# Optimization experiments

Measured on AMD Instinct MI355X. Metric: run time of the kernel, lower is better.

Reference implementation:

```python
import jax, jax.numpy as jnp
import numpy as np

NUM_GENS = 1024
N = 8388608

def setup_inputs() -> dict:
    key = jax.random.key(0)
    k1, k2, k3, k4, k5, k6, k7, k8 = jax.random.split(key, 8)
    return {
        "x_gen": jax.random.randint(k1, (N,), 0, NUM_GENS, dtype=jnp.int64 if jax.config.jax_enable_x64 else jnp.int32),
        "x_ix": jax.random.randint(k2, (N,), 0, NUM_GENS, dtype=jnp.int64 if jax.config.jax_enable_x64 else jnp.int32),
        "x_max_clock_speed": jax.random.normal(k3, (N,), dtype=jnp.float32),
        "x_max_tdp": jax.random.normal(k4, (N,), dtype=jnp.float32),
        "gen_map": jax.random.normal(k5, (NUM_GENS,), dtype=jnp.float32),
        "b": jax.random.normal(k6, (), dtype=jnp.float32),
        "c": jax.random.normal(k7, (), dtype=jnp.float32),
        "d": jax.random.normal(k8, (), dtype=jnp.float32),
    }

def reference(x_gen, x_ix, x_max_clock_speed, x_max_tdp, gen_map, b, c, d):
    # sum(one_hot(x_gen, G) * gen_map, 1) is mathematically gen_map[x_gen]
    gathered = jnp.take(gen_map, x_gen, axis=0)  # [N]
    return gathered + c * x_max_clock_speed + d * x_max_tdp
```

## Files before the change

### kernel.cpp

```cpp
#include <hip/hip_runtime.h>


#define NUM_GENS 1024
#define BLOCK 256
#define GRID 1024
#define UNROLL 4

typedef float nfloat4 __attribute__((ext_vector_type(4)));
typedef int   nint4   __attribute__((ext_vector_type(4)));

__device__ __forceinline__ nfloat4 stage_compute(const float* s_map, float c, float d,
                                                 nint4 g, nfloat4 a, nfloat4 b) {
    nfloat4 o;
    o.x = s_map[g.x] + c * a.x + d * b.x;
    o.y = s_map[g.y] + c * a.y + d * b.y;
    o.z = s_map[g.z] + c * a.z + d * b.z;
    o.w = s_map[g.w] + c * a.w + d * b.w;
    return o;
}

__global__ __launch_bounds__(BLOCK, 4)
void Model_64364379898151_kernel(const int* __restrict__ x_gen,
                                 const float* __restrict__ x_clock,
                                 const float* __restrict__ x_tdp,
                                 const float* __restrict__ gen_map,
                                 const float* __restrict__ c_ptr,
                                 const float* __restrict__ d_ptr,
                                 float* __restrict__ out,
                                 int n_vec)
{
    __shared__ float s_map[NUM_GENS];
    ((float4*)s_map)[threadIdx.x] = ((const float4*)gen_map)[threadIdx.x];
    __syncthreads();

    const float c = c_ptr[0];
    const float d = d_ptr[0];

    const int stride = GRID * BLOCK;
    const int idx = blockIdx.x * BLOCK + threadIdx.x;

    const nint4*   g4 = (const nint4*)  x_gen;
    const nfloat4* c4 = (const nfloat4*)x_clock;
    const nfloat4* t4 = (const nfloat4*)x_tdp;
    nfloat4*       o4 = (nfloat4*)      out;

    if (n_vec == 8 * stride) {
        const int j0 = idx;
        const int j1 = idx + 1 * stride;
        const int j2 = idx + 2 * stride;
        const int j3 = idx + 3 * stride;
        const int j4 = idx + 4 * stride;
        const int j5 = idx + 5 * stride;
        const int j6 = idx + 6 * stride;
        const int j7 = idx + 7 * stride;

        nint4   gA0 = __builtin_nontemporal_load(g4 + j0);
        nint4   gA1 = __builtin_nontemporal_load(g4 + j1);
        nint4   gA2 = __builtin_nontemporal_load(g4 + j2);
        nint4   gA3 = __builtin_nontemporal_load(g4 + j3);
        nfloat4 aA0 = __builtin_nontemporal_load(c4 + j0);
        nfloat4 aA1 = __builtin_nontemporal_load(c4 + j1);
        nfloat4 aA2 = __builtin_nontemporal_load(c4 + j2);
        nfloat4 aA3 = __builtin_nontemporal_load(c4 + j3);
        nfloat4 bA0 = __builtin_nontemporal_load(t4 + j0);
        nfloat4 bA1 = __builtin_nontemporal_load(t4 + j1);
        nfloat4 bA2 = __builtin_nontemporal_load(t4 + j2);
        nfloat4 bA3 = __builtin_nontemporal_load(t4 + j3);
        nint4   gB0 = __builtin_nontemporal_load(g4 + j4);
        nint4   gB1 = __builtin_nontemporal_load(g4 + j5);
        nint4   gB2 = __builtin_nontemporal_load(g4 + j6);
        nint4   gB3 = __builtin_nontemporal_load(g4 + j7);
        nfloat4 aB0 = __builtin_nontemporal_load(c4 + j4);
        nfloat4 aB1 = __builtin_nontemporal_load(c4 + j5);
        nfloat4 aB2 = __builtin_nontemporal_load(c4 + j6);
        nfloat4 aB3 = __builtin_nontemporal_load(c4 + j7);
        nfloat4 bB0 = __builtin_nontemporal_load(t4 + j4);
        nfloat4 bB1 = __builtin_nontemporal_load(t4 + j5);
        nfloat4 bB2 = __builtin_nontemporal_load(t4 + j6);
        nfloat4 bB3 = __builtin_nontemporal_load(t4 + j7);

        __builtin_nontemporal_store(stage_compute(s_map, c, d, gA0, aA0, bA0), o4 + j0);
        __builtin_nontemporal_store(stage_compute(s_map, c, d, gA1, aA1, bA1), o4 + j1);
        __builtin_nontemporal_store(stage_compute(s_map, c, d, gA2, aA2, bA2), o4 + j2);
        __builtin_nontemporal_store(stage_compute(s_map, c, d, gA3, aA3, bA3), o4 + j3);
        __builtin_nontemporal_store(stage_compute(s_map, c, d, gB0, aB0, bB0), o4 + j4);
        __builtin_nontemporal_store(stage_compute(s_map, c, d, gB1, aB1, bB1), o4 + j5);
        __builtin_nontemporal_store(stage_compute(s_map, c, d, gB2, aB2, bB2), o4 + j6);
        __builtin_nontemporal_store(stage_compute(s_map, c, d, gB3, aB3, bB3), o4 + j7);
    } else {
        for (int i = idx; i < n_vec; i += stride) {
            nint4   g  = __builtin_nontemporal_load(g4 + i);
            nfloat4 cs = __builtin_nontemporal_load(c4 + i);
            nfloat4 td = __builtin_nontemporal_load(t4 + i);
            __builtin_nontemporal_store(stage_compute(s_map, c, d, g, cs, td), o4 + i);
        }
    }
}

extern "C" void kernel_launch(void* const* d_in, const int* in_sizes, int n_in,
                              void* d_out, int out_size, void* d_ws, size_t ws_size,
                              hipStream_t stream) {
    const int*   x_gen   = (const int*)  d_in[0];
    const float* x_clock = (const float*)d_in[2];
    const float* x_tdp   = (const float*)d_in[3];
    const float* gen_map = (const float*)d_in[4];
    const float* c_ptr   = (const float*)d_in[6];
    const float* d_ptr   = (const float*)d_in[7];
    float* out = (float*)d_out;

    const int n = in_sizes[0];
    const int n_vec = n / 4;

    Model_64364379898151_kernel<<<GRID, BLOCK, 0, stream>>>(
        x_gen, x_clock, x_tdp, gen_map, c_ptr, d_ptr, out, n_vec);
}
```

Baseline: 157.4 us.

## Switch to contiguous per-block chunks with XCD-aware block remapping and doubled grid

Doubles the grid and gives each block one contiguous chunk of 1024 vec4 groups, replacing the grid-strided layout where each thread handled eight strided groups. A swizzle maps block IDs so consecutive hardware blocks, which are dispatched round-robin across the 8 XCDs, land on distinct contiguous regions, aiming for better DRAM/L2 locality per XCD. Each thread now issues 12 loads instead of 24, trading per-thread memory-level parallelism for more resident blocks.

```diff
diff --git a/kernel.cpp b/kernel.cpp
--- a/kernel.cpp
+++ b/kernel.cpp
@@ -3,8 +3,8 @@
 
 #define NUM_GENS 1024
 #define BLOCK 256
-#define GRID 1024
-#define UNROLL 4
+#define GRID 2048
+#define GROUPS_PER_BLOCK 1024
 
 typedef float nfloat4 __attribute__((ext_vector_type(4)));
 typedef int   nint4   __attribute__((ext_vector_type(4)));
@@ -36,58 +36,41 @@
     const float c = c_ptr[0];
     const float d = d_ptr[0];
 
-    const int stride = GRID * BLOCK;
-    const int idx = blockIdx.x * BLOCK + threadIdx.x;
-
     const nint4*   g4 = (const nint4*)  x_gen;
     const nfloat4* c4 = (const nfloat4*)x_clock;
     const nfloat4* t4 = (const nfloat4*)x_tdp;
     nfloat4*       o4 = (nfloat4*)      out;
 
-    if (n_vec == 8 * stride) {
-        const int j0 = idx;
-        const int j1 = idx + 1 * stride;
-        const int j2 = idx + 2 * stride;
-        const int j3 = idx + 3 * stride;
-        const int j4 = idx + 4 * stride;
-        const int j5 = idx + 5 * stride;
-        const int j6 = idx + 6 * stride;
-        const int j7 = idx + 7 * stride;
+    if (n_vec == GRID * GROUPS_PER_BLOCK) {
+        const int b       = blockIdx.x;
+        const int logical = (b & 7) * (GRID / 8) + (b >> 3);
+        const int base    = logical * GROUPS_PER_BLOCK + (int)threadIdx.x;
 
-        nint4   gA0 = __builtin_nontemporal_load(g4 + j0);
-        nint4   gA1 = __builtin_nontemporal_load(g4 + j1);
-        nint4   gA2 = __builtin_nontemporal_load(g4 + j2);
-        nint4   gA3 = __builtin_nontemporal_load(g4 + j3);
-        nfloat4 aA0 = __builtin_nontemporal_load(c4 + j0);
-        nfloat4 aA1 = __builtin_nontemporal_load(c4 + j1);
-        nfloat4 aA2 = __builtin_nontemporal_load(c4 + j2);
-        nfloat4 aA3 = __builtin_nontemporal_load(c4 + j3);
-        nfloat4 bA0 = __builtin_nontemporal_load(t4 + j0);
-        nfloat4 bA1 = __builtin_nontemporal_load(t4 + j1);
-        nfloat4 bA2 = __builtin_nontemporal_load(t4 + j2);
-        nfloat4 bA3 = __builtin_nontemporal_load(t4 + j3);
-        nint4   gB0 = __builtin_nontemporal_load(g4 + j4);
-        nint4   gB1 = __builtin_nontemporal_load(g4 + j5);
-        nint4   gB2 = __builtin_nontemporal_load(g4 + j6);
-        nint4   gB3 = __builtin_nontemporal_load(g4 + j7);
-        nfloat4 aB0 = __builtin_nontemporal_load(c4 + j4);
-        nfloat4 aB1 = __builtin_nontemporal_load(c4 + j5);
-        nfloat4 aB2 = __builtin_nontemporal_load(c4 + j6);
-        nfloat4 aB3 = __builtin_nontemporal_load(c4 + j7);
-        nfloat4 bB0 = __builtin_nontemporal_load(t4 + j4);
-        nfloat4 bB1 = __builtin_nontemporal_load(t4 + j5);
-        nfloat4 bB2 = __builtin_nontemporal_load(t4 + j6);
-        nfloat4 bB3 = __builtin_nontemporal_load(t4 + j7);
+        const int j0 = base;
+        const int j1 = base + 1 * BLOCK;
+        const int j2 = base + 2 * BLOCK;
+        const int j3 = base + 3 * BLOCK;
 
-        __builtin_nontemporal_store(stage_compute(s_map, c, d, gA0, aA0, bA0), o4 + j0);
-        __builtin_nontemporal_store(stage_compute(s_map, c, d, gA1, aA1, bA1), o4 + j1);
-        __builtin_nontemporal_store(stage_compute(s_map, c, d, gA2, aA2, bA2), o4 + j2);
-        __builtin_nontemporal_store(stage_compute(s_map, c, d, gA3, aA3, bA3), o4 + j3);
-        __builtin_nontemporal_store(stage_compute(s_map, c, d, gB0, aB0, bB0), o4 + j4);
-        __builtin_nontemporal_store(stage_compute(s_map, c, d, gB1, aB1, bB1), o4 + j5);
-        __builtin_nontemporal_store(stage_compute(s_map, c, d, gB2, aB2, bB2), o4 + j6);
-        __builtin_nontemporal_store(stage_compute(s_map, c, d, gB3, aB3, bB3), o4 + j7);
+        nint4   g0 = __builtin_nontemporal_load(g4 + j0);
+        nint4   g1 = __builtin_nontemporal_load(g4 + j1);
+        nint4   g2 = __builtin_nontemporal_load(g4 + j2);
+        nint4   g3 = __builtin_nontemporal_load(g4 + j3);
+        nfloat4 a0 = __builtin_nontemporal_load(c4 + j0);
+        nfloat4 a1 = __builtin_nontemporal_load(c4 + j1);
+        nfloat4 a2 = __builtin_nontemporal_load(c4 + j2);
+        nfloat4 a3 = __builtin_nontemporal_load(c4 + j3);
+        nfloat4 b0 = __builtin_nontemporal_load(t4 + j0);
+        nfloat4 b1 = __builtin_nontemporal_load(t4 + j1);
+        nfloat4 b2 = __builtin_nontemporal_load(t4 + j2);
+        nfloat4 b3 = __builtin_nontemporal_load(t4 + j3);
+
+        __builtin_nontemporal_store(stage_compute(s_map, c, d, g0, a0, b0), o4 + j0);
+        __builtin_nontemporal_store(stage_compute(s_map, c, d, g1, a1, b1), o4 + j1);
+        __builtin_nontemporal_store(stage_compute(s_map, c, d, g2, a2, b2), o4 + j2);
+        __builtin_nontemporal_store(stage_compute(s_map, c, d, g3, a3, b3), o4 + j3);
     } else {
+        const int idx    = blockIdx.x * BLOCK + threadIdx.x;
+        const int stride = GRID * BLOCK;
         for (int i = idx; i < n_vec; i += stride) {
             nint4   g  = __builtin_nontemporal_load(g4 + i);
             nfloat4 cs = __builtin_nontemporal_load(c4 + i);
```

Result: no change. 157.3 us (-0.0%).
